# Performance work log

Measured on AMD Instinct MI355X. Metric: run time of the kernel, lower is better.

## Reference

```python
import jax, jax.numpy as jnp
import numpy as np

H, D, DK, DV = 8, 512, 64, 64
B, L = 2, 2048
LN_EPS = 1e-5


def setup_inputs() -> dict:
    key = jax.random.key(0)
    ks = jax.random.split(key, 12)
    q = jax.random.normal(ks[0], (B, L, D), jnp.float32)
    k = jax.random.normal(ks[1], (B, L, D), jnp.float32)
    v = jax.random.normal(ks[2], (B, L, D), jnp.float32)
    mask = jax.random.randint(ks[3], (H * B, L, L), 0, 2) > 0
    sq = np.sqrt(2.0 / (D + DK)).astype(np.float32)
    sv = np.sqrt(2.0 / (D + DV)).astype(np.float32)
    Wq = jax.random.normal(ks[4], (H * DK, D), jnp.float32) * sq
    Wk = jax.random.normal(ks[5], (H * DK, D), jnp.float32) * sq
    Wv = jax.random.normal(ks[6], (H * DV, D), jnp.float32) * sv
    xav = np.sqrt(2.0 / (H * DV + D)).astype(np.float32)
    Wfc = jax.random.normal(ks[7], (D, H * DV), jnp.float32) * xav
    bfc = jnp.zeros((D,), jnp.float32)
    gamma = jnp.ones((D,), jnp.float32)
    beta = jnp.zeros((D,), jnp.float32)
    return {"q": q, "k": k, "v": v, "mask": mask, "Wq": Wq, "Wk": Wk,
            "Wv": Wv, "Wfc": Wfc, "bfc": bfc, "gamma": gamma, "beta": beta}


def reference(q, k, v, mask, Wq, Wk, Wv, Wfc, bfc, gamma, beta):
    # dropout in eval mode (identity)
    temperature = jnp.sqrt(jnp.asarray(DK, q.dtype))
    residual = q
    # projections -> (H, B, L, dk/dv), matching permute(2,0,1,3)
    qh = (q @ Wq.T).reshape(B, L, H, DK).transpose(2, 0, 1, 3)
    kh = (k @ Wk.T).reshape(B, L, H, DK).transpose(2, 0, 1, 3)
    vh = (v @ Wv.T).reshape(B, L, H, DV).transpose(2, 0, 1, 3)
    attn = jnp.einsum('hbqd,hbkd->hbqk', qh, kh) / temperature
    m = mask.reshape(H, B, L, L)
    attn = jnp.where(m, jnp.asarray(-1e10, attn.dtype), attn)
    attn = jax.nn.softmax(attn, axis=-1)
    out = jnp.einsum('hbqk,hbkd->hbqd', attn, vh)  # (H,B,L,DV)
    out = out.transpose(1, 2, 0, 3).reshape(B, L, H * DV)
    out = out @ Wfc.T + bfc
    x = out + residual
    mu = jnp.mean(x, axis=-1, keepdims=True)
    var = jnp.var(x, axis=-1, keepdims=True)
    return gamma * (x - mu) * jax.lax.rsqrt(var + LN_EPS) + beta
```

## Files before the change

kernel.cpp:

```cpp
#include <hip/hip_runtime.h>
#include <hip/hip_bf16.h>
#include <cmath>
#include <cstdint>

#define H_ 8
#define B_ 2
#define L_ 2048
#define D_ 512
#define SPLIT_ 4

typedef __attribute__((ext_vector_type(8))) short short8_t;
typedef __attribute__((ext_vector_type(4))) float float4_t;
typedef __attribute__((ext_vector_type(4))) unsigned short ushort4_t;
typedef __attribute__((ext_vector_type(2))) unsigned int uint2_t;
typedef __attribute__((ext_vector_type(4))) unsigned int uint4_t;

__device__ __forceinline__ unsigned short f2bf(float f) {
  union { float f; unsigned u; } v; v.f = f;
  unsigned r = v.u + 0x7fffu + ((v.u >> 16) & 1u);
  return (unsigned short)(r >> 16);
}

__device__ __forceinline__ unsigned pack8(unsigned long long x) {
  x |= x >> 4; x |= x >> 2; x |= x >> 1;
  x &= 0x0101010101010101ULL;
  return (unsigned)((x * 0x0102040810204080ULL) >> 56);
}

__global__ __launch_bounds__(256)
void cvt_w(const float* __restrict__ wq, const float* __restrict__ wk,
           const float* __restrict__ wv, const float* __restrict__ wfc,
           unsigned short* __restrict__ wqb, unsigned short* __restrict__ wkb,
           unsigned short* __restrict__ wvb, unsigned short* __restrict__ wfcb) {
  int i = (blockIdx.x * 256 + threadIdx.x) * 4;
  const float* src[4] = {wq, wk, wv, wfc};
  unsigned short* dst[4] = {wqb, wkb, wvb, wfcb};
#pragma unroll
  for (int m = 0; m < 4; m++) {
    float4_t a = *(const float4_t*)(src[m] + i);
    ushort4_t o;
    o[0] = f2bf(a[0]); o[1] = f2bf(a[1]); o[2] = f2bf(a[2]); o[3] = f2bf(a[3]);
    *(ushort4_t*)(dst[m] + i) = o;
  }
}

__global__ __launch_bounds__(512)
void proj_gemm(const float* __restrict__ q, const float* __restrict__ k,
               const float* __restrict__ v,
               const unsigned short* __restrict__ wqb, const unsigned short* __restrict__ wkb,
               const unsigned short* __restrict__ wvb,
               unsigned short* __restrict__ Qp, unsigned short* __restrict__ Kp,
               unsigned short* __restrict__ Vt) {
  __shared__ unsigned short As[128][72];
  __shared__ unsigned short Bs[64][72];
  const int tid = threadIdx.x, lane = tid & 63, wave = tid >> 6;
  const int g = lane >> 4, qi = lane & 15;
  const int m0 = blockIdx.x * 128, n0 = blockIdx.y * 64;
  const int z = blockIdx.z;
  const float* A = (z == 0) ? q : (z == 1) ? k : v;
  const unsigned short* W = (z == 0) ? wqb : (z == 1) ? wkb : wvb;

  float4_t acc[4] = {};
  const int ar = tid >> 2, ac = (tid & 3) * 16;
  const int br = tid >> 3, bc = (tid & 7) * 8;

  for (int kt = 0; kt < 512; kt += 64) {
    const float* src = A + (size_t)(m0 + ar) * 512 + kt + ac;
    float4_t f0 = *(const float4_t*)(src);
    float4_t f1 = *(const float4_t*)(src + 4);
    float4_t f2 = *(const float4_t*)(src + 8);
    float4_t f3 = *(const float4_t*)(src + 12);
    short8_t s0, s1;
    s0[0] = f2bf(f0[0]); s0[1] = f2bf(f0[1]); s0[2] = f2bf(f0[2]); s0[3] = f2bf(f0[3]);
    s0[4] = f2bf(f1[0]); s0[5] = f2bf(f1[1]); s0[6] = f2bf(f1[2]); s0[7] = f2bf(f1[3]);
    s1[0] = f2bf(f2[0]); s1[1] = f2bf(f2[1]); s1[2] = f2bf(f2[2]); s1[3] = f2bf(f2[3]);
    s1[4] = f2bf(f3[0]); s1[5] = f2bf(f3[1]); s1[6] = f2bf(f3[2]); s1[7] = f2bf(f3[3]);
    *(short8_t*)(&As[ar][ac]) = s0;
    *(short8_t*)(&As[ar][ac + 8]) = s1;
    *(short8_t*)(&Bs[br][bc]) = *(const short8_t*)(W + (size_t)(n0 + br) * 512 + kt + bc);
    __syncthreads();
#pragma unroll
    for (int kk = 0; kk < 2; kk++) {
      const int krow = kk * 32 + g * 8;
      short8_t a = *(const short8_t*)(&As[wave * 16 + qi][krow]);
#pragma unroll
      for (int n = 0; n < 4; n++) {
        short8_t b = *(const short8_t*)(&Bs[n * 16 + qi][krow]);
        acc[n] = __builtin_amdgcn_mfma_f32_16x16x32_bf16(a, b, acc[n], 0, 0, 0);
      }
    }
    __syncthreads();
  }

  const int gmb = m0 + wave * 16 + g * 4;
#pragma unroll
  for (int n = 0; n < 4; n++) {
    int gn = n0 + n * 16 + qi;
    int h = gn >> 6, d = gn & 63;
    if (z == 2) {
      int bb = gmb >> 11, l = gmb & 2047;
      ushort4_t o;
#pragma unroll
      for (int r = 0; r < 4; r++) o[r] = f2bf(acc[n][r]);
      *(ushort4_t*)(Vt + ((size_t)(h * B_ + bb) * 64 + d) * L_ + l) = o;
    } else {
      float sc = (z == 0) ? 0.125f : 1.0f;
      unsigned short* O = (z == 0) ? Qp : Kp;
#pragma unroll
      for (int r = 0; r < 4; r++) {
        int gm = gmb + r;
        int bb = gm >> 11, l = gm & 2047;
        O[((size_t)(h * B_ + bb) * L_ + l) * 64 + d] = f2bf(acc[n][r] * sc);
      }
    }
  }
}

template<int MS>
__device__ __forceinline__ void attn_body(
    const unsigned short* __restrict__ Qp, const unsigned short* __restrict__ Kp,
    const unsigned short* __restrict__ Vt, const unsigned char* __restrict__ mask,
    float* __restrict__ Opart, float* __restrict__ MLpart,
    unsigned short (*Ks)[72], unsigned short (*Vs)[72], unsigned int (*Ps)[36]) {
  const int tid = threadIdx.x, lane = tid & 63, wave = tid >> 6;
  const int g = lane >> 4, qi = lane & 15;
  const int hb = blockIdx.y;
  const int sp = blockIdx.z;
  const int k_begin = sp * (L_ / SPLIT_), k_end = k_begin + L_ / SPLIT_;
  const int qg0 = blockIdx.x * 64 + wave * 16;
  const int qg = qg0 + qi;
  const size_t base = (size_t)hb * (L_ * 64);

  const size_t mrowoff = ((size_t)hb * L_ + qg0 + (lane >> 2)) * L_;
  const unsigned char* mb1 = mask + mrowoff + (lane & 3) * 16;
  const unsigned* mb4 = (const unsigned*)mask + mrowoff + (lane & 3) * 16;

  short8_t qf[2];
#pragma unroll
  for (int kk = 0; kk < 2; kk++)
    qf[kk] = *(const short8_t*)(Qp + base + (size_t)qg * 64 + kk * 32 + g * 8);

  float4_t o[4] = {};
  float mrun = -INFINITY, lrun = 0.f;
  const int sr = tid >> 3, sc = (tid & 7) * 8;
  const int srcA = qi * 4;

  for (int k0 = k_begin; k0 < k_end; k0 += 64) {
    unsigned fb;
    if (MS == 1) {
      uint4_t x = *(const uint4_t*)(mb1 + k0);
      unsigned long long lo = ((unsigned long long)x[1] << 32) | x[0];
      unsigned long long hi = ((unsigned long long)x[3] << 32) | x[2];
      fb = pack8(lo) | (pack8(hi) << 8);
    } else {
      fb = 0;
#pragma unroll
      for (int j = 0; j < 4; j++) {
        uint4_t x = *(const uint4_t*)(mb4 + k0 + j * 4);
        fb |= (((unsigned)(x[0] != 0)) | ((unsigned)(x[1] != 0) << 1) |
               ((unsigned)(x[2] != 0) << 2) | ((unsigned)(x[3] != 0) << 3)) << (j * 4);
      }
    }
    unsigned nib[4];
#pragma unroll
    for (int t = 0; t < 4; t++)
      nib[t] = ((unsigned)__shfl((int)fb, srcA + t, 64) >> (g * 4)) & 0xFu;

#pragma unroll
    for (int i = 0; i < 2; i++) {
      int r = sr + i * 32;
      *(short8_t*)(&Ks[r][sc]) = *(const short8_t*)(Kp + base + (size_t)(k0 + r) * 64 + sc);
      *(short8_t*)(&Vs[r][sc]) = *(const short8_t*)(Vt + base + (size_t)r * L_ + k0 + sc);
    }
    __syncthreads();

    float4_t st[4] = {};
#pragma unroll
    for (int kk = 0; kk < 2; kk++) {
      const int krow = kk * 32 + g * 8;
#pragma unroll
      for (int t = 0; t < 4; t++) {
        short8_t a = *(const short8_t*)(&Ks[t * 16 + qi][krow]);
        st[t] = __builtin_amdgcn_mfma_f32_16x16x32_bf16(a, qf[kk], st[t], 0, 0, 0);
      }
    }

    float tmax = -INFINITY;
#pragma unroll
    for (int t = 0; t < 4; t++)
#pragma unroll
      for (int r = 0; r < 4; r++) {
        if ((nib[t] >> r) & 1u) st[t][r] = -1e10f;
        tmax = fmaxf(tmax, st[t][r]);
      }
    tmax = fmaxf(tmax, __shfl_xor(tmax, 16, 64));
    tmax = fmaxf(tmax, __shfl_xor(tmax, 32, 64));

    float nm = fmaxf(mrun, tmax);
    float fac = __expf(mrun - nm);
    mrun = nm;

    float psum = 0.f;
    unsigned w8[4][2];
#pragma unroll
    for (int t = 0; t < 4; t++) {
      float p0 = __expf(st[t][0] - nm);
      float p1 = __expf(st[t][1] - nm);
      float p2 = __expf(st[t][2] - nm);
      float p3 = __expf(st[t][3] - nm);
      psum += (p0 + p1) + (p2 + p3);
      w8[t][0] = (unsigned)f2bf(p0) | ((unsigned)f2bf(p1) << 16);
      w8[t][1] = (unsigned)f2bf(p2) | ((unsigned)f2bf(p3) << 16);
    }
    psum += __shfl_xor(psum, 16, 64);
    psum += __shfl_xor(psum, 32, 64);
    lrun = lrun * fac + psum;
#pragma unroll
    for (int n2 = 0; n2 < 4; n2++)
#pragma unroll
      for (int r = 0; r < 4; r++) o[n2][r] *= fac;

#pragma unroll
    for (int t = 0; t < 4; t++) {
      uint2_t w2; w2[0] = w8[t][0]; w2[1] = w8[t][1];
      *(uint2_t*)(&Ps[qi][t * 8 + g * 2]) = w2;
    }
#pragma unroll
    for (int s = 0; s < 2; s++) {
      short8_t pb = *(const short8_t*)(&Ps[qi][s * 16 + g * 4]);
#pragma unroll
      for (int n2 = 0; n2 < 4; n2++) {
        short8_t a = *(const short8_t*)(&Vs[n2 * 16 + qi][s * 32 + g * 8]);
        o[n2] = __builtin_amdgcn_mfma_f32_16x16x32_bf16(a, pb, o[n2], 0, 0, 0);
      }
    }
    __syncthreads();
  }

  const size_t pb = (((size_t)sp * 16 + hb) * L_ + qg) * 64;
#pragma unroll
  for (int n2 = 0; n2 < 4; n2++)
    *(float4_t*)(Opart + pb + n2 * 16 + g * 4) = o[n2];
  if (lane < 16) {
    float* ml = MLpart + (((size_t)sp * 16 + hb) * L_ + qg) * 2;
    ml[0] = mrun; ml[1] = lrun;
  }
}

__global__ __launch_bounds__(256)
void attn_split(const unsigned short* __restrict__ Qp, const unsigned short* __restrict__ Kp,
                const unsigned short* __restrict__ Vt, const unsigned char* __restrict__ mask,
                float* __restrict__ Opart, float* __restrict__ MLpart) {
  __shared__ unsigned short Ks[64][72];
  __shared__ unsigned short Vs[64][72];
  __shared__ unsigned int PsAll[4][16][36];
  const int wave = threadIdx.x >> 6;
  unsigned probe = ((const unsigned*)mask)[threadIdx.x & 63];
  if (__any(probe > 1u))
    attn_body<1>(Qp, Kp, Vt, mask, Opart, MLpart, Ks, Vs, PsAll[wave]);
  else
    attn_body<4>(Qp, Kp, Vt, mask, Opart, MLpart, Ks, Vs, PsAll[wave]);
}

__global__ __launch_bounds__(256)
void attn_combine(const float* __restrict__ Opart, const float* __restrict__ MLpart,
                  unsigned short* __restrict__ Y) {
  int gid = blockIdx.x * 256 + threadIdx.x;
  int dvc = (gid & 7) * 8;
  int hbq = gid >> 3;
  int hb = hbq >> 11, qq = hbq & 2047;
  int h = hb >> 1, bb = hb & 1;
  float m[SPLIT_], l[SPLIT_];
  float M = -INFINITY;
#pragma unroll
  for (int s = 0; s < SPLIT_; s++) {
    const float* ml = MLpart + (((size_t)s * 16 + hb) * L_ + qq) * 2;
    m[s] = ml[0]; l[s] = ml[1];
    M = fmaxf(M, m[s]);
  }
  float denom = 0.f, e[SPLIT_];
#pragma unroll
  for (int s = 0; s < SPLIT_; s++) { e[s] = __expf(m[s] - M); denom += l[s] * e[s]; }
  float inv = 1.0f / denom;
  float acc[8] = {};
#pragma unroll
  for (int s = 0; s < SPLIT_; s++) {
    const float* p = Opart + (((size_t)s * 16 + hb) * L_ + qq) * 64 + dvc;
    float4_t a0 = *(const float4_t*)(p);
    float4_t a1 = *(const float4_t*)(p + 4);
    float w = e[s] * inv;
#pragma unroll
    for (int j = 0; j < 4; j++) { acc[j] += a0[j] * w; acc[j + 4] += a1[j] * w; }
  }
  short8_t ov;
#pragma unroll
  for (int j = 0; j < 8; j++) ov[j] = (short)f2bf(acc[j]);
  *(short8_t*)(Y + ((size_t)(bb * L_ + qq)) * 512 + h * 64 + dvc) = ov;
}

__global__ __launch_bounds__(512)
void fc_gemm(const unsigned short* __restrict__ Yb, const unsigned short* __restrict__ wfcb,
             const float* __restrict__ resid, const float* __restrict__ bfc,
             float* __restrict__ out) {
  __shared__ unsigned short As[128][72];
  __shared__ unsigned short Bs[64][72];
  const int tid = threadIdx.x, lane = tid & 63, wave = tid >> 6;
  const int g = lane >> 4, qi = lane & 15;
  const int m0 = blockIdx.x * 128, n0 = blockIdx.y * 64;
  float4_t acc[4] = {};
  const int ar = tid >> 2, ac = (tid & 3) * 16;
  const int br = tid >> 3, bc = (tid & 7) * 8;

  for (int kt = 0; kt < 512; kt += 64) {
    const unsigned short* src = Yb + (size_t)(m0 + ar) * 512 + kt + ac;
    *(short8_t*)(&As[ar][ac]) = *(const short8_t*)(src);
    *(short8_t*)(&As[ar][ac + 8]) = *(const short8_t*)(src + 8);
    *(short8_t*)(&Bs[br][bc]) = *(const short8_t*)(wfcb + (size_t)(n0 + br) * 512 + kt + bc);
    __syncthreads();
#pragma unroll
    for (int kk = 0; kk < 2; kk++) {
      const int krow = kk * 32 + g * 8;
      short8_t a = *(const short8_t*)(&As[wave * 16 + qi][krow]);
#pragma unroll
      for (int n = 0; n < 4; n++) {
        short8_t b = *(const short8_t*)(&Bs[n * 16 + qi][krow]);
        acc[n] = __builtin_amdgcn_mfma_f32_16x16x32_bf16(a, b, acc[n], 0, 0, 0);
      }
    }
    __syncthreads();
  }

  const int gmb = m0 + wave * 16 + g * 4;
#pragma unroll
  for (int n = 0; n < 4; n++) {
    int gn = n0 + n * 16 + qi;
    float bv = bfc[gn];
#pragma unroll
    for (int r = 0; r < 4; r++) {
      int gm = gmb + r;
      out[(size_t)gm * 512 + gn] = acc[n][r] + bv + resid[(size_t)gm * 512 + gn];
    }
  }
}

__global__ __launch_bounds__(256)
void ln_kernel(float* __restrict__ Z, const float* __restrict__ gamma,
               const float* __restrict__ beta) {
  const int row = blockIdx.x * 4 + (threadIdx.x >> 6);
  const int lane = threadIdx.x & 63;
  float* zp = Z + (size_t)row * 512 + lane * 8;
  float4_t x0 = *(const float4_t*)(zp);
  float4_t x1 = *(const float4_t*)(zp + 4);
  float s = 0.f, s2 = 0.f;
#pragma unroll
  for (int j = 0; j < 4; j++) { s += x0[j] + x1[j]; s2 += x0[j] * x0[j] + x1[j] * x1[j]; }
#pragma unroll
  for (int mm = 1; mm < 64; mm <<= 1) { s += __shfl_xor(s, mm, 64); s2 += __shfl_xor(s2, mm, 64); }
  float mu = s * (1.f / 512.f);
  float var = s2 * (1.f / 512.f) - mu * mu;
  float inv = rsqrtf(var + 1e-5f);
  float4_t g0 = *(const float4_t*)(gamma + lane * 8);
  float4_t g1 = *(const float4_t*)(gamma + lane * 8 + 4);
  float4_t b0 = *(const float4_t*)(beta + lane * 8);
  float4_t b1 = *(const float4_t*)(beta + lane * 8 + 4);
#pragma unroll
  for (int j = 0; j < 4; j++) {
    x0[j] = g0[j] * (x0[j] - mu) * inv + b0[j];
    x1[j] = g1[j] * (x1[j] - mu) * inv + b1[j];
  }
  *(float4_t*)(zp) = x0;
  *(float4_t*)(zp + 4) = x1;
}

extern "C" void kernel_launch(void* const* d_in, const int* in_sizes, int n_in,
                              void* d_out, int out_size, void* d_ws, size_t ws_size,
                              hipStream_t stream) {
  const float* q   = (const float*)d_in[0];
  const float* k   = (const float*)d_in[1];
  const float* v   = (const float*)d_in[2];
  const unsigned char* mask = (const unsigned char*)d_in[3];
  const float* Wq  = (const float*)d_in[4];
  const float* Wk  = (const float*)d_in[5];
  const float* Wv  = (const float*)d_in[6];
  const float* Wfc = (const float*)d_in[7];
  const float* bfc = (const float*)d_in[8];
  const float* gamma = (const float*)d_in[9];
  const float* beta  = (const float*)d_in[10];
  float* out = (float*)d_out;

  char* ws = (char*)d_ws;
  unsigned short* wqb  = (unsigned short*)(ws);
  unsigned short* wkb  = wqb + 262144;
  unsigned short* wvb  = wkb + 262144;
  unsigned short* wfcb = wvb + 262144;
  unsigned short* Qp   = wfcb + 262144;
  unsigned short* Kp   = Qp + 2097152;
  unsigned short* Vt   = Kp + 2097152;
  unsigned short* Y    = Vt + 2097152;
  float* Opart         = (float*)(Y + 2097152);
  float* MLpart        = Opart + (size_t)SPLIT_ * 16 * L_ * 64;

  cvt_w<<<256, 256, 0, stream>>>(Wq, Wk, Wv, Wfc, wqb, wkb, wvb, wfcb);
  proj_gemm<<<dim3(32, 8, 3), 512, 0, stream>>>(q, k, v, wqb, wkb, wvb, Qp, Kp, Vt);
  attn_split<<<dim3(32, 16, SPLIT_), 256, 0, stream>>>(Qp, Kp, Vt, mask, Opart, MLpart);
  attn_combine<<<1024, 256, 0, stream>>>(Opart, MLpart, Y);
  fc_gemm<<<dim3(32, 8), 512, 0, stream>>>(Y, wfcb, q, bfc, out);
  ln_kernel<<<1024, 256, 0, stream>>>(out, gamma, beta);
}
```

Measured before the change: 149.4 us.

## Prefetch K/V/mask tiles into registers, fuse weight conversion into projection GEMM

The attention loop now loads the next K/V tile and mask bits into registers while the current tile is being computed, instead of loading and immediately stalling before the barrier. The Wq/Wk/Wv bf16 conversion moves out of the separate cvt_w pass and into the projection GEMM's shared-memory staging, so only Wfc is still pre-converted. The hand-written rounding is replaced with the HIP __float2bfloat16 intrinsic. Fused conversion re-reads fp32 weights per block (more bytes and conversions), and the register prefetch raises register pressure.

```diff
diff --git a/kernel.cpp b/kernel.cpp
--- a/kernel.cpp
+++ b/kernel.cpp
@@ -15,10 +15,13 @@
 typedef __attribute__((ext_vector_type(2))) unsigned int uint2_t;
 typedef __attribute__((ext_vector_type(4))) unsigned int uint4_t;
 
-__device__ __forceinline__ unsigned short f2bf(float f) {
-  union { float f; unsigned u; } v; v.f = f;
-  unsigned r = v.u + 0x7fffu + ((v.u >> 16) & 1u);
-  return (unsigned short)(r >> 16);
+__device__ __forceinline__ unsigned short bf16u(float f) {
+  union { __hip_bfloat16 b; unsigned short u; } c;
+  c.b = __float2bfloat16(f);
+  return c.u;
+}
+__device__ __forceinline__ unsigned bf16x2(float lo, float hi) {
+  return (unsigned)bf16u(lo) | ((unsigned)bf16u(hi) << 16);
 }
 
 __device__ __forceinline__ unsigned pack8(unsigned long long x) {
@@ -28,27 +31,19 @@
 }
 
 __global__ __launch_bounds__(256)
-void cvt_w(const float* __restrict__ wq, const float* __restrict__ wk,
-           const float* __restrict__ wv, const float* __restrict__ wfc,
-           unsigned short* __restrict__ wqb, unsigned short* __restrict__ wkb,
-           unsigned short* __restrict__ wvb, unsigned short* __restrict__ wfcb) {
+void cvt_w(const float* __restrict__ wfc, unsigned short* __restrict__ wfcb) {
   int i = (blockIdx.x * 256 + threadIdx.x) * 4;
-  const float* src[4] = {wq, wk, wv, wfc};
-  unsigned short* dst[4] = {wqb, wkb, wvb, wfcb};
-#pragma unroll
-  for (int m = 0; m < 4; m++) {
-    float4_t a = *(const float4_t*)(src[m] + i);
-    ushort4_t o;
-    o[0] = f2bf(a[0]); o[1] = f2bf(a[1]); o[2] = f2bf(a[2]); o[3] = f2bf(a[3]);
-    *(ushort4_t*)(dst[m] + i) = o;
-  }
+  float4_t a = *(const float4_t*)(wfc + i);
+  ushort4_t o;
+  o[0] = bf16u(a[0]); o[1] = bf16u(a[1]); o[2] = bf16u(a[2]); o[3] = bf16u(a[3]);
+  *(ushort4_t*)(wfcb + i) = o;
 }
 
 __global__ __launch_bounds__(512)
 void proj_gemm(const float* __restrict__ q, const float* __restrict__ k,
                const float* __restrict__ v,
-               const unsigned short* __restrict__ wqb, const unsigned short* __restrict__ wkb,
-               const unsigned short* __restrict__ wvb,
+               const float* __restrict__ wq, const float* __restrict__ wk,
+               const float* __restrict__ wv,
                unsigned short* __restrict__ Qp, unsigned short* __restrict__ Kp,
                unsigned short* __restrict__ Vt) {
   __shared__ unsigned short As[128][72];
@@ -58,7 +53,7 @@
   const int m0 = blockIdx.x * 128, n0 = blockIdx.y * 64;
   const int z = blockIdx.z;
   const float* A = (z == 0) ? q : (z == 1) ? k : v;
-  const unsigned short* W = (z == 0) ? wqb : (z == 1) ? wkb : wvb;
+  const float* W = (z == 0) ? wq : (z == 1) ? wk : wv;
 
   float4_t acc[4] = {};
   const int ar = tid >> 2, ac = (tid & 3) * 16;
@@ -71,13 +66,19 @@
     float4_t f2 = *(const float4_t*)(src + 8);
     float4_t f3 = *(const float4_t*)(src + 12);
     short8_t s0, s1;
-    s0[0] = f2bf(f0[0]); s0[1] = f2bf(f0[1]); s0[2] = f2bf(f0[2]); s0[3] = f2bf(f0[3]);
-    s0[4] = f2bf(f1[0]); s0[5] = f2bf(f1[1]); s0[6] = f2bf(f1[2]); s0[7] = f2bf(f1[3]);
-    s1[0] = f2bf(f2[0]); s1[1] = f2bf(f2[1]); s1[2] = f2bf(f2[2]); s1[3] = f2bf(f2[3]);
-    s1[4] = f2bf(f3[0]); s1[5] = f2bf(f3[1]); s1[6] = f2bf(f3[2]); s1[7] = f2bf(f3[3]);
+    s0[0] = bf16u(f0[0]); s0[1] = bf16u(f0[1]); s0[2] = bf16u(f0[2]); s0[3] = bf16u(f0[3]);
+    s0[4] = bf16u(f1[0]); s0[5] = bf16u(f1[1]); s0[6] = bf16u(f1[2]); s0[7] = bf16u(f1[3]);
+    s1[0] = bf16u(f2[0]); s1[1] = bf16u(f2[1]); s1[2] = bf16u(f2[2]); s1[3] = bf16u(f2[3]);
+    s1[4] = bf16u(f3[0]); s1[5] = bf16u(f3[1]); s1[6] = bf16u(f3[2]); s1[7] = bf16u(f3[3]);
     *(short8_t*)(&As[ar][ac]) = s0;
     *(short8_t*)(&As[ar][ac + 8]) = s1;
-    *(short8_t*)(&Bs[br][bc]) = *(const short8_t*)(W + (size_t)(n0 + br) * 512 + kt + bc);
+    const float* wsrc = W + (size_t)(n0 + br) * 512 + kt + bc;
+    float4_t w0 = *(const float4_t*)(wsrc);
+    float4_t w1 = *(const float4_t*)(wsrc + 4);
+    short8_t sw;
+    sw[0] = bf16u(w0[0]); sw[1] = bf16u(w0[1]); sw[2] = bf16u(w0[2]); sw[3] = bf16u(w0[3]);
+    sw[4] = bf16u(w1[0]); sw[5] = bf16u(w1[1]); sw[6] = bf16u(w1[2]); sw[7] = bf16u(w1[3]);
+    *(short8_t*)(&Bs[br][bc]) = sw;
     __syncthreads();
 #pragma unroll
     for (int kk = 0; kk < 2; kk++) {
@@ -101,7 +102,7 @@
       int bb = gmb >> 11, l = gmb & 2047;
       ushort4_t o;
 #pragma unroll
-      for (int r = 0; r < 4; r++) o[r] = f2bf(acc[n][r]);
+      for (int r = 0; r < 4; r++) o[r] = bf16u(acc[n][r]);
       *(ushort4_t*)(Vt + ((size_t)(h * B_ + bb) * 64 + d) * L_ + l) = o;
     } else {
       float sc = (z == 0) ? 0.125f : 1.0f;
@@ -110,7 +111,7 @@
       for (int r = 0; r < 4; r++) {
         int gm = gmb + r;
         int bb = gm >> 11, l = gm & 2047;
-        O[((size_t)(h * B_ + bb) * L_ + l) * 64 + d] = f2bf(acc[n][r] * sc);
+        O[((size_t)(h * B_ + bb) * L_ + l) * 64 + d] = bf16u(acc[n][r] * sc);
       }
     }
   }
@@ -145,8 +146,14 @@
   const int sr = tid >> 3, sc = (tid & 7) * 8;
   const int srcA = qi * 4;
 
-  for (int k0 = k_begin; k0 < k_end; k0 += 64) {
-    unsigned fb;
+  short8_t kr0, kr1, vr0, vr1;
+  unsigned fb;
+  {
+    const int k0 = k_begin;
+    kr0 = *(const short8_t*)(Kp + base + (size_t)(k0 + sr) * 64 + sc);
+    kr1 = *(const short8_t*)(Kp + base + (size_t)(k0 + sr + 32) * 64 + sc);
+    vr0 = *(const short8_t*)(Vt + base + (size_t)sr * L_ + k0 + sc);
+    vr1 = *(const short8_t*)(Vt + base + (size_t)(sr + 32) * L_ + k0 + sc);
     if (MS == 1) {
       uint4_t x = *(const uint4_t*)(mb1 + k0);
       unsigned long long lo = ((unsigned long long)x[1] << 32) | x[0];
@@ -161,18 +168,42 @@
                ((unsigned)(x[2] != 0) << 2) | ((unsigned)(x[3] != 0) << 3)) << (j * 4);
       }
     }
+  }
+
+  for (int k0 = k_begin; k0 < k_end; k0 += 64) {
+    *(short8_t*)(&Ks[sr][sc]) = kr0;
+    *(short8_t*)(&Ks[sr + 32][sc]) = kr1;
+    *(short8_t*)(&Vs[sr][sc]) = vr0;
+    *(short8_t*)(&Vs[sr + 32][sc]) = vr1;
+    unsigned fb_cur = fb;
+    __syncthreads();
+
+    if (k0 + 64 < k_end) {
+      const int kn = k0 + 64;
+      kr0 = *(const short8_t*)(Kp + base + (size_t)(kn + sr) * 64 + sc);
+      kr1 = *(const short8_t*)(Kp + base + (size_t)(kn + sr + 32) * 64 + sc);
+      vr0 = *(const short8_t*)(Vt + base + (size_t)sr * L_ + kn + sc);
+      vr1 = *(const short8_t*)(Vt + base + (size_t)(sr + 32) * L_ + kn + sc);
+      if (MS == 1) {
+        uint4_t x = *(const uint4_t*)(mb1 + kn);
+        unsigned long long lo = ((unsigned long long)x[1] << 32) | x[0];
+        unsigned long long hi = ((unsigned long long)x[3] << 32) | x[2];
+        fb = pack8(lo) | (pack8(hi) << 8);
+      } else {
+        fb = 0;
+#pragma unroll
+        for (int j = 0; j < 4; j++) {
+          uint4_t x = *(const uint4_t*)(mb4 + kn + j * 4);
+          fb |= (((unsigned)(x[0] != 0)) | ((unsigned)(x[1] != 0) << 1) |
+                 ((unsigned)(x[2] != 0) << 2) | ((unsigned)(x[3] != 0) << 3)) << (j * 4);
+        }
+      }
+    }
+
     unsigned nib[4];
 #pragma unroll
     for (int t = 0; t < 4; t++)
-      nib[t] = ((unsigned)__shfl((int)fb, srcA + t, 64) >> (g * 4)) & 0xFu;
-
-#pragma unroll
-    for (int i = 0; i < 2; i++) {
-      int r = sr + i * 32;
-      *(short8_t*)(&Ks[r][sc]) = *(const short8_t*)(Kp + base + (size_t)(k0 + r) * 64 + sc);
-      *(short8_t*)(&Vs[r][sc]) = *(const short8_t*)(Vt + base + (size_t)r * L_ + k0 + sc);
-    }
-    __syncthreads();
+      nib[t] = ((unsigned)__shfl((int)fb_cur, srcA + t, 64) >> (g * 4)) & 0xFu;
 
     float4_t st[4] = {};
 #pragma unroll
@@ -209,8 +240,8 @@
       float p2 = __expf(st[t][2] - nm);
       float p3 = __expf(st[t][3] - nm);
       psum += (p0 + p1) + (p2 + p3);
-      w8[t][0] = (unsigned)f2bf(p0) | ((unsigned)f2bf(p1) << 16);
-      w8[t][1] = (unsigned)f2bf(p2) | ((unsigned)f2bf(p3) << 16);
+      w8[t][0] = bf16x2(p0, p1);
+      w8[t][1] = bf16x2(p2, p3);
     }
     psum += __shfl_xor(psum, 16, 64);
     psum += __shfl_xor(psum, 32, 64);
@@ -294,7 +325,7 @@
   }
   short8_t ov;
 #pragma unroll
-  for (int j = 0; j < 8; j++) ov[j] = (short)f2bf(acc[j]);
+  for (int j = 0; j < 8; j++) ov[j] = bf16u(acc[j]);
   *(short8_t*)(Y + ((size_t)(bb * L_ + qq)) * 512 + h * 64 + dvc) = ov;
 }
 
@@ -389,10 +420,7 @@
   float* out = (float*)d_out;
 
   char* ws = (char*)d_ws;
-  unsigned short* wqb  = (unsigned short*)(ws);
-  unsigned short* wkb  = wqb + 262144;
-  unsigned short* wvb  = wkb + 262144;
-  unsigned short* wfcb = wvb + 262144;
+  unsigned short* wfcb = (unsigned short*)(ws);
   unsigned short* Qp   = wfcb + 262144;
   unsigned short* Kp   = Qp + 2097152;
   unsigned short* Vt   = Kp + 2097152;
@@ -400,8 +428,8 @@
   float* Opart         = (float*)(Y + 2097152);
   float* MLpart        = Opart + (size_t)SPLIT_ * 16 * L_ * 64;
 
-  cvt_w<<<256, 256, 0, stream>>>(Wq, Wk, Wv, Wfc, wqb, wkb, wvb, wfcb);
-  proj_gemm<<<dim3(32, 8, 3), 512, 0, stream>>>(q, k, v, wqb, wkb, wvb, Qp, Kp, Vt);
+  cvt_w<<<256, 256, 0, stream>>>(Wfc, wfcb);
+  proj_gemm<<<dim3(32, 8, 3), 512, 0, stream>>>(q, k, v, Wq, Wk, Wv, Qp, Kp, Vt);
   attn_split<<<dim3(32, 16, SPLIT_), 256, 0, stream>>>(Qp, Kp, Vt, mask, Opart, MLpart);
   attn_combine<<<1024, 256, 0, stream>>>(Opart, MLpart, Y);
   fc_gemm<<<dim3(32, 8), 512, 0, stream>>>(Y, wfcb, q, bfc, out);
```

New measurement: 136.7 us. 8.5% less time.
